# Performance work log

Measured on AMD Instinct MI355X. Metric: run time of the kernel, lower is better.

Reference implementation:

```python
import jax, jax.numpy as jnp
import numpy as np

N_NODES = 100000
IN_C, HID_C, OUT_C = 128, 64, 5
NEG_SLOPE = 0.01  # F.leaky_relu default


def gcn_conv(x, W, b, src_sl, dst_sl, norm, n_nodes):
    """PyG GCNConv: h = D^{-1/2}(A+I)D^{-1/2} (x W) + b.
    src_sl/dst_sl already include self-loops; norm is the per-edge coefficient."""
    h = x @ W                              # [N, out]
    msg = h[src_sl] * norm[:, None]        # [E+N, out] gather + scale
    agg = jax.ops.segment_sum(msg, dst_sl, num_segments=n_nodes)
    return agg + b


def setup_inputs() -> dict:
    key = jax.random.key(0)
    ks = jax.random.split(key, 8)
    n, e = N_NODES, 1600000
    x = jax.random.normal(ks[0], (n, IN_C), dtype=jnp.float32)
    edge_index = jax.random.randint(ks[1], (2, e), 0, n, dtype=jnp.int64)
    idx = jax.random.randint(ks[2], (20000,), 0, n, dtype=jnp.int64)
    # Glorot-ish init for GCNConv weights, kaiming-ish for MLP
    W0 = jax.random.normal(ks[3], (IN_C, HID_C), dtype=jnp.float32) * (1.0 / np.sqrt(IN_C))
    b0 = jnp.zeros((HID_C,), dtype=jnp.float32)
    W1 = jax.random.normal(ks[4], (HID_C, HID_C), dtype=jnp.float32) * (1.0 / np.sqrt(HID_C))
    b1 = jnp.zeros((HID_C,), dtype=jnp.float32)
    Wm = jax.random.normal(ks[5], (HID_C, OUT_C), dtype=jnp.float32) * (1.0 / np.sqrt(HID_C))
    bm = jnp.zeros((OUT_C,), dtype=jnp.float32)
    return {"x": x, "edge_index": edge_index, "idx": idx,
            "W0": W0, "b0": b0, "W1": W1, "b1": b1, "Wm": Wm, "bm": bm}


def reference(x, edge_index, idx, W0, b0, W1, b1, Wm, bm):
    n = x.shape[0]
    src, dst = edge_index[0], edge_index[1]
    loops = jnp.arange(n, dtype=edge_index.dtype)
    src_sl = jnp.concatenate([src, loops])
    dst_sl = jnp.concatenate([dst, loops])
    # symmetric normalization with self-loops (gcn_norm)
    deg = jax.ops.segment_sum(jnp.ones_like(dst_sl, dtype=x.dtype), dst_sl, num_segments=n)
    dinv = jnp.where(deg > 0, jax.lax.rsqrt(deg), 0.0)
    norm = dinv[src_sl] * dinv[dst_sl]     # [E+N]

    h = jax.nn.leaky_relu(gcn_conv(x, W0, b0, src_sl, dst_sl, norm, n), NEG_SLOPE)
    h = jax.nn.leaky_relu(gcn_conv(h, W1, b1, src_sl, dst_sl, norm, n), NEG_SLOPE)

    h_sel = h[idx]                          # index_select on node dim
    out = jax.nn.sigmoid(h_sel @ Wm + bm)
    return (h_sel, out)
```

## Files before the change

### kernel.cpp

```cpp
#include <hip/hip_runtime.h>
#include <hip/hip_fp16.h>
#include <math.h>


#define NPART 64
#define MAXB 2048

typedef _Float16 h8 __attribute__((ext_vector_type(8)));
typedef float f4v __attribute__((ext_vector_type(4)));

__device__ __forceinline__ float lrelu(float x) { return x > 0.0f ? x : 0.01f * x; }


__global__ __launch_bounds__(1024) void k_part_hist(const int* __restrict__ dst, int E,
                                                    int B, int* __restrict__ phist) {
    __shared__ int scnt[MAXB];
    int t = threadIdx.x, p = blockIdx.x;
    for (int i = t; i < B; i += 1024) scnt[i] = 0;
    __syncthreads();
    int ep = (((E + NPART - 1) / NPART) + 3) & ~3;
    int beg = p * ep, endi = min(E, beg + ep);
    int cnt4 = (endi - beg) >> 2;
    for (int i = t; i < cnt4; i += 1024) {
        int4 d = *(const int4*)(dst + beg + i * 4);
        atomicAdd(&scnt[d.x >> 6], 1);
        atomicAdd(&scnt[d.y >> 6], 1);
        atomicAdd(&scnt[d.z >> 6], 1);
        atomicAdd(&scnt[d.w >> 6], 1);
    }
    int rem = (endi - beg) & 3;
    if (t < rem) atomicAdd(&scnt[dst[beg + cnt4 * 4 + t] >> 6], 1);
    __syncthreads();
    for (int i = t; i < B; i += 1024) phist[i * NPART + p] = scnt[i];
}

__global__ __launch_bounds__(1024) void k_part_scatter(const int* __restrict__ src,
                                                       const int* __restrict__ dst, int E,
                                                       int B, const int* __restrict__ pbase,
                                                       int* __restrict__ esA) {
    __shared__ int sbase[MAXB];
    int t = threadIdx.x, p = blockIdx.x;
    for (int i = t; i < B; i += 1024) sbase[i] = pbase[i * NPART + p];
    __syncthreads();
    int ep = (((E + NPART - 1) / NPART) + 3) & ~3;
    int beg = p * ep, endi = min(E, beg + ep);
    int cnt4 = (endi - beg) >> 2;
    for (int i = t; i < cnt4; i += 1024) {
        int e = beg + i * 4;
        int4 d = *(const int4*)(dst + e);
        int4 s = *(const int4*)(src + e);
        int p0 = atomicAdd(&sbase[d.x >> 6], 1);
        int p1 = atomicAdd(&sbase[d.y >> 6], 1);
        int p2 = atomicAdd(&sbase[d.z >> 6], 1);
        int p3 = atomicAdd(&sbase[d.w >> 6], 1);
        esA[p0] = ((d.x & 63) << 24) | s.x;
        esA[p1] = ((d.y & 63) << 24) | s.y;
        esA[p2] = ((d.z & 63) << 24) | s.z;
        esA[p3] = ((d.w & 63) << 24) | s.w;
    }
    int rem = (endi - beg) & 3;
    if (t < rem) {
        int e = beg + cnt4 * 4 + t;
        int d = dst[e];
        int pos = atomicAdd(&sbase[d >> 6], 1);
        esA[pos] = ((d & 63) << 24) | src[e];
    }
}


__global__ void k_blocksum(const int* __restrict__ cnt, int N, int* __restrict__ bsum) {
    __shared__ int sm[256];
    int b = blockIdx.x, t = threadIdx.x;
    int base = b * 1024 + t * 4;
    int s = 0;
#pragma unroll
    for (int i = 0; i < 4; ++i) { int j = base + i; if (j < N) s += cnt[j]; }
    sm[t] = s; __syncthreads();
    for (int off = 128; off > 0; off >>= 1) {
        if (t < off) sm[t] += sm[t + off];
        __syncthreads();
    }
    if (t == 0) bsum[b] = sm[0];
}

__global__ void k_scan_bsum(int* __restrict__ bsum, int nb, int* __restrict__ offN) {
    __shared__ int sm[1024];
    int t = threadIdx.x;
    int v = (t < nb) ? bsum[t] : 0;
    sm[t] = v; __syncthreads();
    for (int d = 1; d < 1024; d <<= 1) {
        int add = (t >= d) ? sm[t - d] : 0;
        __syncthreads();
        sm[t] += add;
        __syncthreads();
    }
    if (t < nb) bsum[t] = sm[t] - v;
    if (t == nb - 1) *offN = sm[t];
}

__global__ void k_scan_block(const int* __restrict__ cnt, const int* __restrict__ bsum,
                             int* __restrict__ off, int N) {
    __shared__ int sm[256];
    int b = blockIdx.x, t = threadIdx.x;
    int base = b * 1024 + t * 4;
    int v[4];
#pragma unroll
    for (int i = 0; i < 4; ++i) { int j = base + i; v[i] = (j < N) ? cnt[j] : 0; }
    int tsum = v[0] + v[1] + v[2] + v[3];
    sm[t] = tsum; __syncthreads();
    for (int d = 1; d < 256; d <<= 1) {
        int val = (t >= d) ? sm[t - d] : 0;
        __syncthreads();
        sm[t] += val;
        __syncthreads();
    }
    int run = sm[t] - tsum + bsum[b];
#pragma unroll
    for (int i = 0; i < 4; ++i) {
        int j = base + i;
        if (j < N) off[j] = run;
        run += v[i];
    }
}


__global__ __launch_bounds__(256) void k_bsort(const int* __restrict__ pbase, int BP,
                                               const int* __restrict__ esA,
                                               int* __restrict__ esB,
                                               int* __restrict__ off,
                                               float* __restrict__ dinv,
                                               int N, int E) {
    __shared__ int hcnt[64];
    __shared__ int hoff[64];
    int t = threadIdx.x, b = blockIdx.x;
    int start = pbase[b * NPART];
    int endi  = pbase[min((b + 1) * NPART, BP)];
    int cnt = endi - start;

    if (t < 64) hcnt[t] = 0;
    __syncthreads();
    for (int i = t * 4; i < cnt; i += 1024) {
#pragma unroll
        for (int c = 0; c < 4; ++c)
            if (i + c < cnt) atomicAdd(&hcnt[(esA[start + i + c] >> 24) & 63], 1);
    }
    __syncthreads();

    if (t < 64) {
        int c = hcnt[t];
        int v = c;
#pragma unroll
        for (int d = 1; d < 64; d <<= 1) {
            int u = __shfl_up(v, d);
            if (t >= d) v += u;
        }
        int pos = start + (v - c);
        hoff[t] = pos;
        int g = b * 64 + t;
        if (g < N) {
            off[g] = pos;
            dinv[g] = rsqrtf((float)c + 1.0f);
        }
        if (g == N - 1) off[N] = E;
    }
    __syncthreads();
    if (t < 64) hcnt[t] = hoff[t];
    __syncthreads();

    for (int i = t * 4; i < cnt; i += 1024) {
#pragma unroll
        for (int c = 0; c < 4; ++c)
            if (i + c < cnt) {
                int v = esA[start + i + c];
                int pos = atomicAdd(&hcnt[(v >> 24) & 63], 1);
                esB[pos] = v & 0xFFFFFF;
            }
    }
}


template <int K, typename AT>
__global__ __launch_bounds__(256) void k_gemm(const AT* __restrict__ A,
                                              const float* __restrict__ W,
                                              const float* __restrict__ dinv,
                                              __half* __restrict__ hout, int N) {
    constexpr int ASTR = K + 8;
    __shared__ _Float16 a16[64 * ASTR];
    __shared__ _Float16 wt16[64 * ASTR];
    int t = threadIdx.x, lane = t & 63, wv = t >> 6;
    int rowBase = blockIdx.x * 64;

#pragma unroll
    for (int i = 0; i < K / 16; ++i) {
        int g = i * 256 + t;
        int r = g / (K / 4), kq = g % (K / 4);
        int gr = rowBase + r; if (gr >= N) gr = N - 1;
        _Float16* p = a16 + r * ASTR + kq * 4;
        if constexpr (sizeof(AT) == 4) {
            float4 v = *(const float4*)((const float*)A + (size_t)gr * K + kq * 4);
            *(__half2*)(p)     = __floats2half2_rn(v.x, v.y);
            *(__half2*)(p + 2) = __floats2half2_rn(v.z, v.w);
        } else {
            *(uint2*)p = *(const uint2*)((const __half*)A + (size_t)gr * K + kq * 4);
        }
    }
#pragma unroll
    for (int i = 0; i < K / 16; ++i) {
        int g = i * 256 + t;
        int k = g >> 4, nq = g & 15;
        float4 v = *(const float4*)(W + (size_t)k * 64 + nq * 4);
        wt16[(nq * 4 + 0) * ASTR + k] = (_Float16)v.x;
        wt16[(nq * 4 + 1) * ASTR + k] = (_Float16)v.y;
        wt16[(nq * 4 + 2) * ASTR + k] = (_Float16)v.z;
        wt16[(nq * 4 + 3) * ASTR + k] = (_Float16)v.w;
    }
    __syncthreads();

    int m = lane & 15, q = lane >> 4;
    f4v acc[4] = {{0,0,0,0},{0,0,0,0},{0,0,0,0},{0,0,0,0}};
    const _Float16* arow = a16 + (wv * 16 + m) * ASTR + q * 8;
#pragma unroll
    for (int kt = 0; kt < K / 32; ++kt) {
        h8 af = *(const h8*)(arow + kt * 32);
#pragma unroll
        for (int nt = 0; nt < 4; ++nt) {
            h8 bf = *(const h8*)(wt16 + (nt * 16 + m) * ASTR + kt * 32 + q * 8);
            acc[nt] = __builtin_amdgcn_mfma_f32_16x16x32_f16(af, bf, acc[nt], 0, 0, 0);
        }
    }

    int r0 = rowBase + wv * 16 + q * 4;
#pragma unroll
    for (int reg = 0; reg < 4; ++reg) {
        int row = r0 + reg;
        if (row >= N) continue;
        float dv = dinv[row];
#pragma unroll
        for (int nt = 0; nt < 4; ++nt)
            hout[(size_t)row * 64 + nt * 16 + m] = (__half)(acc[nt][reg] * dv);
    }
}


__global__ __launch_bounds__(256) void k_agg1(const int* __restrict__ off,
                                              const int* __restrict__ esB,
                                              const float* __restrict__ dinv,
                                              const __half* __restrict__ hs,
                                              const float* __restrict__ b0,
                                              __half* __restrict__ aout, int N) {
    int lane = threadIdx.x & 63;
    int node = (blockIdx.x * blockDim.x + threadIdx.x) >> 6;
    if (node >= N) return;
    int qt = lane >> 4, l16 = lane & 15;
    int beg = off[node], end = off[node + 1];
    float dv = dinv[node];
    float4 b = *(const float4*)(b0 + l16 * 4);

    float ax0 = 0, ay0 = 0, az0 = 0, aw0 = 0;
    float ax1 = 0, ay1 = 0, az1 = 0, aw1 = 0;
    auto ld = [&](int s) { return *(const uint2*)(hs + (size_t)s * 64 + l16 * 4); };
    auto acc4a = [&](uint2 u) {
        float2 f0 = __half22float2(*(__half2*)&u.x);
        float2 f1 = __half22float2(*(__half2*)&u.y);
        ax0 += f0.x; ay0 += f0.y; az0 += f1.x; aw0 += f1.y;
    };
    auto acc4b = [&](uint2 u) {
        float2 f0 = __half22float2(*(__half2*)&u.x);
        float2 f1 = __half22float2(*(__half2*)&u.y);
        ax1 += f0.x; ay1 += f0.y; az1 += f1.x; aw1 += f1.y;
    };
    if (qt == 0) acc4a(ld(node));
    int last = end - 1;
    for (int j = beg + qt; j < end; j += 16) {
        int j1 = min(j + 4, last), j2 = min(j + 8, last), j3 = min(j + 12, last);
        int s0 = esB[j], s1 = esB[j1], s2 = esB[j2], s3 = esB[j3];
        uint2 u0 = ld(s0), u1 = ld(s1), u2 = ld(s2), u3 = ld(s3);
        acc4a(u0);
        if (j + 4 < end)  acc4b(u1);
        if (j + 8 < end)  acc4a(u2);
        if (j + 12 < end) acc4b(u3);
    }
    float ax = ax0 + ax1, ay = ay0 + ay1, az = az0 + az1, aw = aw0 + aw1;

#pragma unroll
    for (int d = 16; d <= 32; d <<= 1) {
        ax += __shfl_xor(ax, d); ay += __shfl_xor(ay, d);
        az += __shfl_xor(az, d); aw += __shfl_xor(aw, d);
    }
    if (qt == 0) {
        float ox = lrelu(ax * dv + b.x), oy = lrelu(ay * dv + b.y);
        float oz = lrelu(az * dv + b.z), ow = lrelu(aw * dv + b.w);
        uint2 u;
        *(__half2*)&u.x = __floats2half2_rn(ox, oy);
        *(__half2*)&u.y = __floats2half2_rn(oz, ow);
        *(uint2*)(aout + (size_t)node * 64 + l16 * 4) = u;
    }
}


__global__ __launch_bounds__(256) void k_aggout(const int* __restrict__ idx,
                                                const int* __restrict__ off,
                                                const int* __restrict__ esB,
                                                const float* __restrict__ dinv,
                                                const __half* __restrict__ hs,
                                                const float* __restrict__ b1,
                                                const float* __restrict__ Wm,
                                                const float* __restrict__ bm,
                                                float* __restrict__ out, int NSEL) {
    int lane = threadIdx.x & 63;
    int wv = (blockIdx.x * blockDim.x + threadIdx.x) >> 6;
    if (wv >= NSEL) return;
    int node = idx[wv];
    int qt = lane >> 4, l16 = lane & 15;
    int beg = off[node], end = off[node + 1];
    float dv = dinv[node];
    float4 b = *(const float4*)(b1 + l16 * 4);

    float ax0 = 0, ay0 = 0, az0 = 0, aw0 = 0;
    float ax1 = 0, ay1 = 0, az1 = 0, aw1 = 0;
    auto ld = [&](int s) { return *(const uint2*)(hs + (size_t)s * 64 + l16 * 4); };
    auto acc4a = [&](uint2 u) {
        float2 f0 = __half22float2(*(__half2*)&u.x);
        float2 f1 = __half22float2(*(__half2*)&u.y);
        ax0 += f0.x; ay0 += f0.y; az0 += f1.x; aw0 += f1.y;
    };
    auto acc4b = [&](uint2 u) {
        float2 f0 = __half22float2(*(__half2*)&u.x);
        float2 f1 = __half22float2(*(__half2*)&u.y);
        ax1 += f0.x; ay1 += f0.y; az1 += f1.x; aw1 += f1.y;
    };
    if (qt == 0) acc4a(ld(node));
    int last = end - 1;
    for (int j = beg + qt; j < end; j += 16) {
        int j1 = min(j + 4, last), j2 = min(j + 8, last), j3 = min(j + 12, last);
        int s0 = esB[j], s1 = esB[j1], s2 = esB[j2], s3 = esB[j3];
        uint2 u0 = ld(s0), u1 = ld(s1), u2 = ld(s2), u3 = ld(s3);
        acc4a(u0);
        if (j + 4 < end)  acc4b(u1);
        if (j + 8 < end)  acc4a(u2);
        if (j + 12 < end) acc4b(u3);
    }
    float ax = ax0 + ax1, ay = ay0 + ay1, az = az0 + az1, aw = aw0 + aw1;

#pragma unroll
    for (int d = 16; d <= 32; d <<= 1) {
        ax += __shfl_xor(ax, d); ay += __shfl_xor(ay, d);
        az += __shfl_xor(az, d); aw += __shfl_xor(aw, d);
    }

    float4 hsel;
    hsel.x = lrelu(ax * dv + b.x); hsel.y = lrelu(ay * dv + b.y);
    hsel.z = lrelu(az * dv + b.z); hsel.w = lrelu(aw * dv + b.w);
    if (qt == 0) *(float4*)(out + (size_t)wv * 64 + l16 * 4) = hsel;

    const float* wr = Wm + (size_t)(4 * l16) * 5;
#pragma unroll
    for (int o = 0; o < 5; ++o) {
        float p = hsel.x * wr[o] + hsel.y * wr[5 + o] +
                  hsel.z * wr[10 + o] + hsel.w * wr[15 + o];
        p += __shfl_xor(p, 1); p += __shfl_xor(p, 2);
        p += __shfl_xor(p, 4); p += __shfl_xor(p, 8);
        if (lane == 0)
            out[(size_t)NSEL * 64 + (size_t)wv * 5 + o] =
                1.0f / (1.0f + expf(-(p + bm[o])));
    }
}

extern "C" void kernel_launch(void* const* d_in, const int* in_sizes, int n_in,
                              void* d_out, int out_size, void* d_ws, size_t ws_size,
                              hipStream_t stream) {
    const float* x   = (const float*)d_in[0];
    const int*   ei  = (const int*)d_in[1];
    const int*   idx = (const int*)d_in[2];
    const float* W0  = (const float*)d_in[3];
    const float* b0  = (const float*)d_in[4];
    const float* W1  = (const float*)d_in[5];
    const float* b1  = (const float*)d_in[6];
    const float* Wm  = (const float*)d_in[7];
    const float* bm  = (const float*)d_in[8];

    int N    = in_sizes[0] / 128;
    int E    = in_sizes[1] / 2;
    int NSEL = in_sizes[2];
    const int* src = ei;
    const int* dst = ei + E;

    int B  = (N + 63) / 64;
    int BP = B * NPART;

    char* w = (char*)d_ws;
    size_t Na  = ((size_t)N + 1023) & ~(size_t)1023;
    size_t Ea  = ((size_t)E + 1023) & ~(size_t)1023;
    size_t BPa = ((size_t)BP + 1023) & ~(size_t)1023;
    float*  dinv  = (float*)w;                w += Na * 4;
    int*    phist = (int*)w;                  w += BPa * 4;
    int*    pbase = (int*)w;                  w += (BPa + 1024) * 4;
    int*    bsum  = (int*)w;                  w += 1024 * 4;
    int*    off   = (int*)w;                  w += (Na + 1024) * 4;
    int*    esA   = (int*)w;                  w += Ea * 4;
    int*    esB   = (int*)w;                  w += Ea * 4;
    __half* hs16  = (__half*)w;               w += (size_t)N * 64 * 2;
    __half* a16g  = (__half*)w;

    int nbp = (BP + 1023) / 1024;

    k_part_hist<<<NPART, 1024, 0, stream>>>(dst, E, B, phist);
    k_blocksum<<<nbp, 256, 0, stream>>>(phist, BP, bsum);
    k_scan_bsum<<<1, 1024, 0, stream>>>(bsum, nbp, pbase + BP);
    k_scan_block<<<nbp, 256, 0, stream>>>(phist, bsum, pbase, BP);
    k_part_scatter<<<NPART, 1024, 0, stream>>>(src, dst, E, B, pbase, esA);
    k_bsort<<<B, 256, 0, stream>>>(pbase, BP, esA, esB, off, dinv, N, E);

    int gemm_blocks = (N + 63) / 64;
    int agg_blocks  = (N + 3) / 4;

    k_gemm<128, float><<<gemm_blocks, 256, 0, stream>>>(x, W0, dinv, hs16, N);
    k_agg1<<<agg_blocks, 256, 0, stream>>>(off, esB, dinv, hs16, b0, a16g, N);
    k_gemm<64, __half><<<gemm_blocks, 256, 0, stream>>>(a16g, W1, dinv, hs16, N);
    k_aggout<<<(NSEL + 3) / 4, 256, 0, stream>>>(idx, off, esB, dinv, hs16, b1, Wm, bm,
                                                 (float*)d_out, NSEL);
}
```

Baseline: 250.8 us.

## Store GEMM output in column-quarter planes and split aggregation by feature quarter

The GEMM now writes the fp16 hidden features as four planes of 16 columns each, so a node's 16-column slice is 32 contiguous bytes. The first aggregation kernel is restructured so each block handles one column quarter for 16 nodes, with 16 edges processed in parallel per wave. The aim is a smaller random-gather footprint per quarter, for better L2 locality. In exchange, edge indices are re-read four times, each wave walks its 4 nodes serially, and the old 4-way unrolled loads are gone. The output kernel is adapted to the new layout, and a redundant duplicated lrelu computation is left in.

```diff
diff --git a/kernel.cpp b/kernel.cpp
--- a/kernel.cpp
+++ b/kernel.cpp
@@ -237,7 +237,7 @@
         float dv = dinv[row];
 #pragma unroll
         for (int nt = 0; nt < 4; ++nt)
-            hout[(size_t)row * 64 + nt * 16 + m] = (__half)(acc[nt][reg] * dv);
+            hout[((size_t)nt * N + row) * 16 + m] = (__half)(acc[nt][reg] * dv);
     }
 }
 
@@ -245,20 +245,77 @@
 __global__ __launch_bounds__(256) void k_agg1(const int* __restrict__ off,
                                               const int* __restrict__ esB,
                                               const float* __restrict__ dinv,
-                                              const __half* __restrict__ hs,
+                                              const __half* __restrict__ hsq,
                                               const float* __restrict__ b0,
                                               __half* __restrict__ aout, int N) {
+    int t = threadIdx.x, lane = t & 63, wv = t >> 6;
+    int q = blockIdx.x & 3;
+    int nodeBase = ((int)(blockIdx.x >> 2) * 4 + wv) * 4;
+    if (nodeBase >= N) return;
+    int eg = lane >> 2, l4 = lane & 3;
+    const __half* hq = hsq + (size_t)q * N * 16 + l4 * 4;
+    float4 b = *(const float4*)(b0 + q * 16 + l4 * 4);
+    int nEnd = min(nodeBase + 4, N);
+
+    for (int node = nodeBase; node < nEnd; ++node) {
+        int beg = off[node], end = off[node + 1];
+        float dv = dinv[node];
+        float ax = 0, ay = 0, az = 0, aw = 0;
+        auto ld = [&](int s) { return *(const uint2*)(hq + (size_t)s * 16); };
+        auto acc4 = [&](uint2 u) {
+            float2 f0 = __half22float2(*(__half2*)&u.x);
+            float2 f1 = __half22float2(*(__half2*)&u.y);
+            ax += f0.x; ay += f0.y; az += f1.x; aw += f1.y;
+        };
+        if (eg == 0) acc4(ld(node));
+        int last = end - 1;
+        for (int j0 = beg; j0 < end; j0 += 16) {
+            int j = j0 + eg;
+            int s = esB[min(j, last)];
+            uint2 u = ld(s);
+            if (j < end) acc4(u);
+        }
+#pragma unroll
+        for (int d = 4; d <= 32; d <<= 1) {
+            ax += __shfl_xor(ax, d); ay += __shfl_xor(ay, d);
+            az += __shfl_xor(az, d); aw += __shfl_xor(aw, d);
+        }
+        if (eg == 0) {
+            float ox = lrelu(ax * dv + b.x), oy = lrelu(ay * dv + b.y);
+            float oz = lrelu(az * dv + b.z), ow = lrelu(az == az ? aw * dv + b.w : 0.0f);
+            oz = lrelu(az * dv + b.z); ow = lrelu(aw * dv + b.w);
+            uint2 u;
+            *(__half2*)&u.x = __floats2half2_rn(ox, oy);
+            *(__half2*)&u.y = __floats2half2_rn(oz, ow);
+            *(uint2*)(aout + (size_t)node * 64 + q * 16 + l4 * 4) = u;
+        }
+    }
+}
+
+
+__global__ __launch_bounds__(256) void k_aggout(const int* __restrict__ idx,
+                                                const int* __restrict__ off,
+                                                const int* __restrict__ esB,
+                                                const float* __restrict__ dinv,
+                                                const __half* __restrict__ hs,
+                                                const float* __restrict__ b1,
+                                                const float* __restrict__ Wm,
+                                                const float* __restrict__ bm,
+                                                float* __restrict__ out,
+                                                int NSEL, int N) {
     int lane = threadIdx.x & 63;
-    int node = (blockIdx.x * blockDim.x + threadIdx.x) >> 6;
-    if (node >= N) return;
+    int wv = (blockIdx.x * blockDim.x + threadIdx.x) >> 6;
+    if (wv >= NSEL) return;
+    int node = idx[wv];
     int qt = lane >> 4, l16 = lane & 15;
     int beg = off[node], end = off[node + 1];
     float dv = dinv[node];
-    float4 b = *(const float4*)(b0 + l16 * 4);
+    float4 b = *(const float4*)(b1 + l16 * 4);
+    const __half* hq = hs + (size_t)(l16 >> 2) * N * 16 + (l16 & 3) * 4;
 
     float ax0 = 0, ay0 = 0, az0 = 0, aw0 = 0;
     float ax1 = 0, ay1 = 0, az1 = 0, aw1 = 0;
-    auto ld = [&](int s) { return *(const uint2*)(hs + (size_t)s * 64 + l16 * 4); };
+    auto ld = [&](int s) { return *(const uint2*)(hq + (size_t)s * 16); };
     auto acc4a = [&](uint2 u) {
         float2 f0 = __half22float2(*(__half2*)&u.x);
         float2 f1 = __half22float2(*(__half2*)&u.y);
@@ -287,66 +344,6 @@
         ax += __shfl_xor(ax, d); ay += __shfl_xor(ay, d);
         az += __shfl_xor(az, d); aw += __shfl_xor(aw, d);
     }
-    if (qt == 0) {
-        float ox = lrelu(ax * dv + b.x), oy = lrelu(ay * dv + b.y);
-        float oz = lrelu(az * dv + b.z), ow = lrelu(aw * dv + b.w);
-        uint2 u;
-        *(__half2*)&u.x = __floats2half2_rn(ox, oy);
-        *(__half2*)&u.y = __floats2half2_rn(oz, ow);
-        *(uint2*)(aout + (size_t)node * 64 + l16 * 4) = u;
-    }
-}
-
-
-__global__ __launch_bounds__(256) void k_aggout(const int* __restrict__ idx,
-                                                const int* __restrict__ off,
-                                                const int* __restrict__ esB,
-                                                const float* __restrict__ dinv,
-                                                const __half* __restrict__ hs,
-                                                const float* __restrict__ b1,
-                                                const float* __restrict__ Wm,
-                                                const float* __restrict__ bm,
-                                                float* __restrict__ out, int NSEL) {
-    int lane = threadIdx.x & 63;
-    int wv = (blockIdx.x * blockDim.x + threadIdx.x) >> 6;
-    if (wv >= NSEL) return;
-    int node = idx[wv];
-    int qt = lane >> 4, l16 = lane & 15;
-    int beg = off[node], end = off[node + 1];
-    float dv = dinv[node];
-    float4 b = *(const float4*)(b1 + l16 * 4);
-
-    float ax0 = 0, ay0 = 0, az0 = 0, aw0 = 0;
-    float ax1 = 0, ay1 = 0, az1 = 0, aw1 = 0;
-    auto ld = [&](int s) { return *(const uint2*)(hs + (size_t)s * 64 + l16 * 4); };
-    auto acc4a = [&](uint2 u) {
-        float2 f0 = __half22float2(*(__half2*)&u.x);
-        float2 f1 = __half22float2(*(__half2*)&u.y);
-        ax0 += f0.x; ay0 += f0.y; az0 += f1.x; aw0 += f1.y;
-    };
-    auto acc4b = [&](uint2 u) {
-        float2 f0 = __half22float2(*(__half2*)&u.x);
-        float2 f1 = __half22float2(*(__half2*)&u.y);
-        ax1 += f0.x; ay1 += f0.y; az1 += f1.x; aw1 += f1.y;
-    };
-    if (qt == 0) acc4a(ld(node));
-    int last = end - 1;
-    for (int j = beg + qt; j < end; j += 16) {
-        int j1 = min(j + 4, last), j2 = min(j + 8, last), j3 = min(j + 12, last);
-        int s0 = esB[j], s1 = esB[j1], s2 = esB[j2], s3 = esB[j3];
-        uint2 u0 = ld(s0), u1 = ld(s1), u2 = ld(s2), u3 = ld(s3);
-        acc4a(u0);
-        if (j + 4 < end)  acc4b(u1);
-        if (j + 8 < end)  acc4a(u2);
-        if (j + 12 < end) acc4b(u3);
-    }
-    float ax = ax0 + ax1, ay = ay0 + ay1, az = az0 + az1, aw = aw0 + aw1;
-
-#pragma unroll
-    for (int d = 16; d <= 32; d <<= 1) {
-        ax += __shfl_xor(ax, d); ay += __shfl_xor(ay, d);
-        az += __shfl_xor(az, d); aw += __shfl_xor(aw, d);
-    }
 
     float4 hsel;
     hsel.x = lrelu(ax * dv + b.x); hsel.y = lrelu(ay * dv + b.y);
@@ -412,11 +409,11 @@
     k_bsort<<<B, 256, 0, stream>>>(pbase, BP, esA, esB, off, dinv, N, E);
 
     int gemm_blocks = (N + 63) / 64;
-    int agg_blocks  = (N + 3) / 4;
+    int agg1_blocks = 4 * ((N + 15) / 16);
 
     k_gemm<128, float><<<gemm_blocks, 256, 0, stream>>>(x, W0, dinv, hs16, N);
-    k_agg1<<<agg_blocks, 256, 0, stream>>>(off, esB, dinv, hs16, b0, a16g, N);
+    k_agg1<<<agg1_blocks, 256, 0, stream>>>(off, esB, dinv, hs16, b0, a16g, N);
     k_gemm<64, __half><<<gemm_blocks, 256, 0, stream>>>(a16g, W1, dinv, hs16, N);
     k_aggout<<<(NSEL + 3) / 4, 256, 0, stream>>>(idx, off, esB, dinv, hs16, b1, Wm, bm,
-                                                 (float*)d_out, NSEL);
-}
+                                                 (float*)d_out, NSEL, N);
+}
```

Measured after the change: 309.5 us. +23.4%, slower.
